# Performance work log

Measured on AMD Instinct MI355X. Metric: run time of the kernel, lower is better.

Reference implementation:

```python
import jax, jax.numpy as jnp
import numpy as np

ITER = 25
SMOOTH = 1e-05


def _maxpool(x, wh, ww):
    # stride-1 'same' max pool over H,W of an NCHW tensor
    return jax.lax.reduce_window(
        x, -jnp.inf, jax.lax.max,
        window_dimensions=(1, 1, wh, ww),
        window_strides=(1, 1, 1, 1),
        padding=[(0, 0), (0, 0), (wh // 2, wh // 2), (ww // 2, ww // 2)])


def soft_erode(img):
    p1 = -_maxpool(-img, 3, 1)
    p2 = -_maxpool(-img, 1, 3)
    return jnp.minimum(p1, p2)


def soft_dilate(img):
    return _maxpool(img, 3, 3)


def soft_open(img):
    return soft_dilate(soft_erode(img))


def soft_skel(img, iter_):
    skel = jax.nn.relu(img - soft_open(img))

    def body(j, carry):
        img, skel = carry
        img = soft_erode(img)
        delta = jax.nn.relu(img - soft_open(img))
        skel = skel + jax.nn.relu(delta - skel * delta)
        return (img, skel)

    _, skel = jax.lax.fori_loop(0, iter_, body, (img, skel))
    return skel


def setup_inputs() -> dict:
    key = jax.random.key(0)
    k1, k2 = jax.random.split(key)
    shape = (32, 1, 1024, 1024)
    target = jax.random.uniform(k1, shape, dtype=jnp.float32)
    inputs = jax.random.uniform(k2, shape, dtype=jnp.float32)
    return {"target": target, "inputs": inputs}


def reference(target, inputs):
    # skeletons computed under no_grad in the original -> stop_gradient
    skel_pred = jax.lax.stop_gradient(soft_skel(inputs, ITER))
    skel_true = jax.lax.stop_gradient(soft_skel(target, ITER))
    tprec = (jnp.sum(skel_pred * target) + SMOOTH) / (jnp.sum(skel_pred) + SMOOTH)
    tsens = (jnp.sum(skel_true * inputs) + SMOOTH) / (jnp.sum(skel_true) + SMOOTH)
    cl_dice = 1.0 - 2.0 * (tprec * tsens) / (tprec + tsens)
    return cl_dice
```

## Files before the change

### kernel.cpp

```cpp
#include <hip/hip_runtime.h>
#include <hip/hip_fp16.h>

#define HH 1024
#define WW 1024
#define NB 32
#define PLANE (HH*WW)
#define RR 118
#define RC 128
typedef unsigned int u32;
typedef unsigned short u16;

static __device__ __forceinline__ u32 pmin(u32 a, u32 b){ u32 d; asm("v_pk_min_f16 %0,%1,%2":"=v"(d):"v"(a),"v"(b)); return d; }
static __device__ __forceinline__ u32 pmax(u32 a, u32 b){ u32 d; asm("v_pk_max_f16 %0,%1,%2":"=v"(d):"v"(a),"v"(b)); return d; }
static __device__ __forceinline__ u32 padd(u32 a, u32 b){ u32 d; asm("v_pk_add_f16 %0,%1,%2":"=v"(d):"v"(a),"v"(b)); return d; }
static __device__ __forceinline__ u32 pmul(u32 a, u32 b){ u32 d; asm("v_pk_mul_f16 %0,%1,%2":"=v"(d):"v"(a),"v"(b)); return d; }
static __device__ __forceinline__ u32 psub(u32 a, u32 b){ u32 d; asm("v_pk_add_f16 %0,%1,%2 neg_lo:[0,1] neg_hi:[0,1]":"=v"(d):"v"(a),"v"(b)); return d; }
static __device__ __forceinline__ float h2f(u32 s){ float f; asm("v_cvt_f32_f16 %0,%1":"=v"(f):"v"(s)); return f; }
static __device__ __forceinline__ u32 cvt2(float a, float b){
    typedef __fp16 h2v __attribute__((ext_vector_type(2)));
    union { h2v h; u32 u; } r; r.h = __builtin_amdgcn_cvt_pkrtz(a,b); return r.u;
}
#define DPP_SHR1(x) ((u32)__builtin_amdgcn_mov_dpp((int)(x), 0x111, 0xf, 0xf, true))
#define DPP_SHL1(x) ((u32)__builtin_amdgcn_mov_dpp((int)(x), 0x101, 0xf, 0xf, true))
#define QNAN2 0x7e007e00u
#define AB(hi,lo) (((lo)>>16)|((hi)<<16))

__global__ __launch_bounds__(256,4) void cldice_fused(const float* __restrict__ inputs,
                                                      const float* __restrict__ target,
                                                      double* __restrict__ acc) {
    __shared__ __align__(16) u16 buf[RR*RC];
    const int tid = threadIdx.x;
    const int bx = blockIdx.x*64, by = blockIdx.y*64;
    const int img = blockIdx.z >> 5, n = blockIdx.z & 31;
    const float* xsrc = (img==0) ? inputs : target;
    const float* wsrc = (img==0) ? target : inputs;
    const float* im = xsrc + (size_t)n*PLANE;
    const bool interior = (bx>=64 && bx<=896 && by>=64 && by<=896);
    const int r0 = tid>>4, c = tid&15;
    const int gx = bx - 32 + 8*c;
    const bool colok = ((unsigned)gx < (unsigned)WW);

    #pragma unroll
    for (int g = 0; g < 8; g++) {
        int r = r0 + g*16;
        if (r < RR) {
            int gy = by - 27 + r;
            uint4 v;
            if (interior || (colok && (unsigned)gy < (unsigned)HH)) {
                const float* p = im + (size_t)gy*WW + gx;
                float4 f0 = *(const float4*)p, f1 = *(const float4*)(p+4);
                v.x = cvt2(f0.x,f0.y); v.y = cvt2(f0.z,f0.w);
                v.z = cvt2(f1.x,f1.y); v.w = cvt2(f1.z,f1.w);
            } else {
                v = make_uint4(QNAN2,QNAN2,QNAN2,QNAN2);
            }
            *(uint4*)&buf[tid*8 + g*2048] = v;
        }
    }
    __syncthreads();

    u32 sk[2][4] = {{0,0,0,0},{0,0,0,0}};
    const int bc0 = 3456 + (tid>>3)*128 + (tid&7)*8;
    const int bc1 = 3456 + ((tid+256)>>3)*128 + (tid&7)*8;

    #pragma unroll 1
    for (int t = 0; t < 26; t++) {
        uint4 st[8];
        #pragma unroll
        for (int g = 0; g < 8; g++) {
            int r = r0 + g*16;
            bool act = (r >= t+1) & (r <= 116-t);
            if (act) {
                int base = tid*8 + g*2048;
                uint4 up = *(const uint4*)&buf[base-RC];
                uint4 md = *(const uint4*)&buf[base];
                uint4 dn = *(const uint4*)&buf[base+RC];
                u32 lfs = DPP_SHR1(md.w);
                u32 rts = DPP_SHL1(md.x);
                u32 vx = pmin(up.x,dn.x), vy = pmin(up.y,dn.y);
                u32 vz = pmin(up.z,dn.z), vw = pmin(up.w,dn.w);
                u32 B1 = AB(md.y,md.x), B2 = AB(md.z,md.y), B3 = AB(md.w,md.z);
                u32 B4 = (md.w>>16)|(rts<<16);
                u32 M0 = (md.x<<16)|(lfs>>16);
                uint4 e;
                e.x = pmin(pmin(vx,md.x), pmin(M0,B1));
                e.y = pmin(pmin(vy,md.y), pmin(B1,B2));
                e.z = pmin(pmin(vz,md.z), pmin(B2,B3));
                e.w = pmin(pmin(vw,md.w), pmin(B3,B4));
                if (!interior) {
                    int gy = by - 27 + r;
                    if (!(colok && (unsigned)gy < (unsigned)HH))
                        e = make_uint4(QNAN2,QNAN2,QNAN2,QNAN2);
                }
                st[g] = e;
            }
        }
        uint4 xs0 = *(const uint4*)&buf[bc0];
        uint4 xs1 = *(const uint4*)&buf[bc1];
        __syncthreads();
        #pragma unroll
        for (int g = 0; g < 8; g++) {
            int r = r0 + g*16;
            if ((r >= t+1) & (r <= 116-t))
                *(uint4*)&buf[tid*8 + g*2048] = st[g];
        }
        __syncthreads();
        #pragma unroll
        for (int j = 0; j < 2; j++) {
            int base = j ? bc1 : bc0;
            uint4 xs = j ? xs1 : xs0;
            uint4 up = *(const uint4*)&buf[base-RC];
            uint4 md = *(const uint4*)&buf[base];
            uint4 dn = *(const uint4*)&buf[base+RC];
            uint4 vm;
            vm.x = pmax(pmax(up.x,dn.x),md.x);
            vm.y = pmax(pmax(up.y,dn.y),md.y);
            vm.z = pmax(pmax(up.z,dn.z),md.z);
            vm.w = pmax(pmax(up.w,dn.w),md.w);
            u32 lfm = DPP_SHR1(vm.w);
            u32 rtm = DPP_SHL1(vm.x);
            if ((tid&7)==0) {
                u32 a = buf[base-RC-1], b = buf[base-1], d2 = buf[base+RC-1];
                lfm = pmax(pmax(a,b),d2) << 16;
            }
            if ((tid&7)==7) {
                u32 a = buf[base-RC+8], b = buf[base+8], d2 = buf[base+RC+8];
                rtm = pmax(pmax(a,b),d2) & 0xffffu;
            }
            u32 B1 = AB(vm.y,vm.x), B2 = AB(vm.z,vm.y), B3 = AB(vm.w,vm.z);
            u32 B4 = (vm.w>>16)|(rtm<<16);
            u32 M0 = (vm.x<<16)|(lfm>>16);
            uint4 d;
            d.x = pmax(pmax(M0,B1), vm.x);
            d.y = pmax(pmax(B1,B2), vm.y);
            d.z = pmax(pmax(B2,B3), vm.z);
            d.w = pmax(pmax(B3,B4), vm.w);
            uint4 dl;
            dl.x = pmax(psub(xs.x,d.x), 0u);
            dl.y = pmax(psub(xs.y,d.y), 0u);
            dl.z = pmax(psub(xs.z,d.z), 0u);
            dl.w = pmax(psub(xs.w,d.w), 0u);
            sk[j][0] = padd(sk[j][0], pmax(psub(dl.x, pmul(sk[j][0],dl.x)), 0u));
            sk[j][1] = padd(sk[j][1], pmax(psub(dl.y, pmul(sk[j][1],dl.y)), 0u));
            sk[j][2] = padd(sk[j][2], pmax(psub(dl.z, pmul(sk[j][2],dl.z)), 0u));
            sk[j][3] = padd(sk[j][3], pmax(psub(dl.w, pmul(sk[j][3],dl.w)), 0u));
        }
    }

    double s0 = 0.0, s1 = 0.0;
    const float* wim = wsrc + (size_t)n*PLANE;
    #pragma unroll
    for (int j = 0; j < 2; j++) {
        int ti = tid + j*256, ty = ti>>3, cx = ti&7;
        const float* p = wim + (size_t)(by+ty)*WW + bx + 8*cx;
        float4 w0 = *(const float4*)p, w1 = *(const float4*)(p+4);
        float f0 = h2f(sk[j][0]&0xffffu), f1 = h2f(sk[j][0]>>16);
        float f2 = h2f(sk[j][1]&0xffffu), f3 = h2f(sk[j][1]>>16);
        float f4 = h2f(sk[j][2]&0xffffu), f5 = h2f(sk[j][2]>>16);
        float f6 = h2f(sk[j][3]&0xffffu), f7 = h2f(sk[j][3]>>16);
        s0 += (double)(f0*w0.x) + (double)(f1*w0.y) + (double)(f2*w0.z) + (double)(f3*w0.w)
            + (double)(f4*w1.x) + (double)(f5*w1.y) + (double)(f6*w1.z) + (double)(f7*w1.w);
        s1 += (double)f0 + (double)f1 + (double)f2 + (double)f3
            + (double)f4 + (double)f5 + (double)f6 + (double)f7;
    }
    #pragma unroll
    for (int off = 32; off > 0; off >>= 1) {
        s0 += __shfl_down(s0, off, 64);
        s1 += __shfl_down(s1, off, 64);
    }
    __syncthreads();
    double* sh = (double*)buf;
    int lane = tid & 63, wid = tid >> 6;
    if (lane == 0) { sh[wid] = s0; sh[4+wid] = s1; }
    __syncthreads();
    if (tid == 0) {
        atomicAdd(&acc[img*2 + 0], sh[0]+sh[1]+sh[2]+sh[3]);
        atomicAdd(&acc[img*2 + 1], sh[4]+sh[5]+sh[6]+sh[7]);
    }
}

__global__ void final_kernel(const double* __restrict__ acc, float* __restrict__ out) {
    double tprec = (acc[0] + 1e-5) / (acc[1] + 1e-5);
    double tsens = (acc[2] + 1e-5) / (acc[3] + 1e-5);
    out[0] = (float)(1.0 - 2.0 * (tprec * tsens) / (tprec + tsens));
}

extern "C" void kernel_launch(void* const* d_in, const int* in_sizes, int n_in,
                              void* d_out, int out_size, void* d_ws, size_t ws_size,
                              hipStream_t stream) {
    const float* target = (const float*)d_in[0];
    const float* inputs = (const float*)d_in[1];
    float* out = (float*)d_out;
    double* acc = (double*)d_ws;

    (void)hipMemsetAsync(acc, 0, 4*sizeof(double), stream);
    dim3 grid(WW/64, HH/64, NB*2);
    cldice_fused<<<grid, dim3(256), 0, stream>>>(inputs, target, acc);
    final_kernel<<<1, 1, 0, stream>>>(acc, out);
}
```

Before: 1.241 ms.

## Double tile height to 128 rows and pad LDS row stride

Grows each block's tile from 64 to 128 output rows, so the 27-row halo on each side is amortized over twice as many outputs and redundant erosion work per pixel drops. The shared-memory row stride is padded to 136 elements, which should reduce bank conflicts. Each thread now keeps 12 staged rows and 4 skeleton accumulators. Launch bounds drop to 3 blocks per CU, trading occupancy and register pressure for less halo recomputation.

```diff
diff --git a/kernel.cpp b/kernel.cpp
--- a/kernel.cpp
+++ b/kernel.cpp
@@ -5,8 +5,8 @@
 #define WW 1024
 #define NB 32
 #define PLANE (HH*WW)
-#define RR 118
-#define RC 128
+#define RR 182
+#define CS 136
 typedef unsigned int u32;
 typedef unsigned short u16;
 
@@ -25,23 +25,24 @@
 #define QNAN2 0x7e007e00u
 #define AB(hi,lo) (((lo)>>16)|((hi)<<16))
 
-__global__ __launch_bounds__(256,4) void cldice_fused(const float* __restrict__ inputs,
+__global__ __launch_bounds__(256,3) void cldice_fused(const float* __restrict__ inputs,
                                                       const float* __restrict__ target,
                                                       double* __restrict__ acc) {
-    __shared__ __align__(16) u16 buf[RR*RC];
+    __shared__ __align__(16) u16 buf[RR*CS];
     const int tid = threadIdx.x;
-    const int bx = blockIdx.x*64, by = blockIdx.y*64;
+    const int bx = blockIdx.x*64, by = blockIdx.y*128;
     const int img = blockIdx.z >> 5, n = blockIdx.z & 31;
     const float* xsrc = (img==0) ? inputs : target;
     const float* wsrc = (img==0) ? target : inputs;
     const float* im = xsrc + (size_t)n*PLANE;
-    const bool interior = (bx>=64 && bx<=896 && by>=64 && by<=896);
+    const bool interior = (bx>=64 && bx<=896 && by>=128 && by<=768);
     const int r0 = tid>>4, c = tid&15;
     const int gx = bx - 32 + 8*c;
     const bool colok = ((unsigned)gx < (unsigned)WW);
-
-    #pragma unroll
-    for (int g = 0; g < 8; g++) {
+    const int rowoff = r0*CS + c*8;
+
+    #pragma unroll
+    for (int g = 0; g < 12; g++) {
         int r = r0 + g*16;
         if (r < RR) {
             int gy = by - 27 + r;
@@ -54,27 +55,31 @@
             } else {
                 v = make_uint4(QNAN2,QNAN2,QNAN2,QNAN2);
             }
-            *(uint4*)&buf[tid*8 + g*2048] = v;
+            *(uint4*)&buf[rowoff + g*16*CS] = v;
         }
     }
     __syncthreads();
 
-    u32 sk[2][4] = {{0,0,0,0},{0,0,0,0}};
-    const int bc0 = 3456 + (tid>>3)*128 + (tid&7)*8;
-    const int bc1 = 3456 + ((tid+256)>>3)*128 + (tid&7)*8;
+    u32 sk[4][4] = {{0,0,0,0},{0,0,0,0},{0,0,0,0},{0,0,0,0}};
+    int bc[4];
+    #pragma unroll
+    for (int j = 0; j < 4; j++) {
+        int ti = tid + j*256;
+        bc[j] = (27 + (ti>>3))*CS + (4 + (ti&7))*8;
+    }
 
     #pragma unroll 1
     for (int t = 0; t < 26; t++) {
-        uint4 st[8];
-        #pragma unroll
-        for (int g = 0; g < 8; g++) {
+        uint4 st[12];
+        #pragma unroll
+        for (int g = 0; g < 12; g++) {
             int r = r0 + g*16;
-            bool act = (r >= t+1) & (r <= 116-t);
+            bool act = (r >= t+1) & (r <= 180-t);
             if (act) {
-                int base = tid*8 + g*2048;
-                uint4 up = *(const uint4*)&buf[base-RC];
+                int base = rowoff + g*16*CS;
+                uint4 up = *(const uint4*)&buf[base-CS];
                 uint4 md = *(const uint4*)&buf[base];
-                uint4 dn = *(const uint4*)&buf[base+RC];
+                uint4 dn = *(const uint4*)&buf[base+CS];
                 u32 lfs = DPP_SHR1(md.w);
                 u32 rts = DPP_SHL1(md.x);
                 u32 vx = pmin(up.x,dn.x), vy = pmin(up.y,dn.y);
@@ -95,23 +100,23 @@
                 st[g] = e;
             }
         }
-        uint4 xs0 = *(const uint4*)&buf[bc0];
-        uint4 xs1 = *(const uint4*)&buf[bc1];
+        uint4 xs[4];
+        #pragma unroll
+        for (int j = 0; j < 4; j++) xs[j] = *(const uint4*)&buf[bc[j]];
         __syncthreads();
         #pragma unroll
-        for (int g = 0; g < 8; g++) {
+        for (int g = 0; g < 12; g++) {
             int r = r0 + g*16;
-            if ((r >= t+1) & (r <= 116-t))
-                *(uint4*)&buf[tid*8 + g*2048] = st[g];
+            if ((r >= t+1) & (r <= 180-t))
+                *(uint4*)&buf[rowoff + g*16*CS] = st[g];
         }
         __syncthreads();
         #pragma unroll
-        for (int j = 0; j < 2; j++) {
-            int base = j ? bc1 : bc0;
-            uint4 xs = j ? xs1 : xs0;
-            uint4 up = *(const uint4*)&buf[base-RC];
+        for (int j = 0; j < 4; j++) {
+            int base = bc[j];
+            uint4 up = *(const uint4*)&buf[base-CS];
             uint4 md = *(const uint4*)&buf[base];
-            uint4 dn = *(const uint4*)&buf[base+RC];
+            uint4 dn = *(const uint4*)&buf[base+CS];
             uint4 vm;
             vm.x = pmax(pmax(up.x,dn.x),md.x);
             vm.y = pmax(pmax(up.y,dn.y),md.y);
@@ -120,11 +125,11 @@
             u32 lfm = DPP_SHR1(vm.w);
             u32 rtm = DPP_SHL1(vm.x);
             if ((tid&7)==0) {
-                u32 a = buf[base-RC-1], b = buf[base-1], d2 = buf[base+RC-1];
+                u32 a = buf[base-CS-1], b = buf[base-1], d2 = buf[base+CS-1];
                 lfm = pmax(pmax(a,b),d2) << 16;
             }
             if ((tid&7)==7) {
-                u32 a = buf[base-RC+8], b = buf[base+8], d2 = buf[base+RC+8];
+                u32 a = buf[base-CS+8], b = buf[base+8], d2 = buf[base+CS+8];
                 rtm = pmax(pmax(a,b),d2) & 0xffffu;
             }
             u32 B1 = AB(vm.y,vm.x), B2 = AB(vm.z,vm.y), B3 = AB(vm.w,vm.z);
@@ -136,10 +141,10 @@
             d.z = pmax(pmax(B2,B3), vm.z);
             d.w = pmax(pmax(B3,B4), vm.w);
             uint4 dl;
-            dl.x = pmax(psub(xs.x,d.x), 0u);
-            dl.y = pmax(psub(xs.y,d.y), 0u);
-            dl.z = pmax(psub(xs.z,d.z), 0u);
-            dl.w = pmax(psub(xs.w,d.w), 0u);
+            dl.x = pmax(psub(xs[j].x,d.x), 0u);
+            dl.y = pmax(psub(xs[j].y,d.y), 0u);
+            dl.z = pmax(psub(xs[j].z,d.z), 0u);
+            dl.w = pmax(psub(xs[j].w,d.w), 0u);
             sk[j][0] = padd(sk[j][0], pmax(psub(dl.x, pmul(sk[j][0],dl.x)), 0u));
             sk[j][1] = padd(sk[j][1], pmax(psub(dl.y, pmul(sk[j][1],dl.y)), 0u));
             sk[j][2] = padd(sk[j][2], pmax(psub(dl.z, pmul(sk[j][2],dl.z)), 0u));
@@ -150,7 +155,7 @@
     double s0 = 0.0, s1 = 0.0;
     const float* wim = wsrc + (size_t)n*PLANE;
     #pragma unroll
-    for (int j = 0; j < 2; j++) {
+    for (int j = 0; j < 4; j++) {
         int ti = tid + j*256, ty = ti>>3, cx = ti&7;
         const float* p = wim + (size_t)(by+ty)*WW + bx + 8*cx;
         float4 w0 = *(const float4*)p, w1 = *(const float4*)(p+4);
@@ -194,7 +199,7 @@
     double* acc = (double*)d_ws;
 
     (void)hipMemsetAsync(acc, 0, 4*sizeof(double), stream);
-    dim3 grid(WW/64, HH/64, NB*2);
+    dim3 grid(WW/64, HH/128, NB*2);
     cldice_fused<<<grid, dim3(256), 0, stream>>>(inputs, target, acc);
     final_kernel<<<1, 1, 0, stream>>>(acc, out);
 }
```

New measurement: 1.263 ms. No clear change (+1.8%).

## Keep erosion tile in registers and exchange only halo rows through LDS

Applied to the files above, without the earlier changes.

Each thread now holds an 8-row strip of the fp16 tile in registers. Only the boundary rows of each strip go through a small double-buffered LDS exchange, which replaces the full-tile shared buffer and one of the two barriers per iteration. The tile grows to 128 output rows with 384 threads, so the vertical halo costs less relative to the useful work. The dilate/skeleton step skips the horizontal halo columns, which frees those threads from that work. The price is higher register pressure (x, e and sk arrays) at 3 blocks per CU, which risks spills or lower occupancy.

```diff
diff --git a/kernel.cpp b/kernel.cpp
--- a/kernel.cpp
+++ b/kernel.cpp
@@ -1,14 +1,10 @@
 #include <hip/hip_runtime.h>
-#include <hip/hip_fp16.h>
 
 #define HH 1024
 #define WW 1024
 #define NB 32
 #define PLANE (HH*WW)
-#define RR 118
-#define RC 128
 typedef unsigned int u32;
-typedef unsigned short u16;
 
 static __device__ __forceinline__ u32 pmin(u32 a, u32 b){ u32 d; asm("v_pk_min_f16 %0,%1,%2":"=v"(d):"v"(a),"v"(b)); return d; }
 static __device__ __forceinline__ u32 pmax(u32 a, u32 b){ u32 d; asm("v_pk_max_f16 %0,%1,%2":"=v"(d):"v"(a),"v"(b)); return d; }
@@ -24,144 +20,142 @@
 #define DPP_SHL1(x) ((u32)__builtin_amdgcn_mov_dpp((int)(x), 0x101, 0xf, 0xf, true))
 #define QNAN2 0x7e007e00u
 #define AB(hi,lo) (((lo)>>16)|((hi)<<16))
+#define QN4 make_uint4(QNAN2,QNAN2,QNAN2,QNAN2)
 
-__global__ __launch_bounds__(256,4) void cldice_fused(const float* __restrict__ inputs,
+static __device__ __forceinline__ uint4 erode_row(uint4 up, uint4 md, uint4 dn){
+    u32 lfs = DPP_SHR1(md.w);
+    u32 rts = DPP_SHL1(md.x);
+    u32 vx = pmin(up.x,dn.x), vy = pmin(up.y,dn.y);
+    u32 vz = pmin(up.z,dn.z), vw = pmin(up.w,dn.w);
+    u32 B1 = AB(md.y,md.x), B2 = AB(md.z,md.y), B3 = AB(md.w,md.z);
+    u32 B4 = (md.w>>16)|(rts<<16);
+    u32 M0 = (md.x<<16)|(lfs>>16);
+    uint4 e;
+    e.x = pmin(pmin(vx,md.x), pmin(M0,B1));
+    e.y = pmin(pmin(vy,md.y), pmin(B1,B2));
+    e.z = pmin(pmin(vz,md.z), pmin(B2,B3));
+    e.w = pmin(pmin(vw,md.w), pmin(B3,B4));
+    return e;
+}
+
+__global__ __launch_bounds__(384,3) void cldice_fused(const float* __restrict__ inputs,
                                                       const float* __restrict__ target,
                                                       double* __restrict__ acc) {
-    __shared__ __align__(16) u16 buf[RR*RC];
+    __shared__ uint4 ex[2][24][2][16];
     const int tid = threadIdx.x;
-    const int bx = blockIdx.x*64, by = blockIdx.y*64;
+    const int s = tid >> 4, c = tid & 15;
+    const int bx = blockIdx.x*64, by = blockIdx.y*128;
     const int img = blockIdx.z >> 5, n = blockIdx.z & 31;
     const float* xsrc = (img==0) ? inputs : target;
     const float* wsrc = (img==0) ? target : inputs;
     const float* im = xsrc + (size_t)n*PLANE;
-    const bool interior = (bx>=64 && bx<=896 && by>=64 && by<=896);
-    const int r0 = tid>>4, c = tid&15;
     const int gx = bx - 32 + 8*c;
     const bool colok = ((unsigned)gx < (unsigned)WW);
+    const int rbase = 8*s;
+    const bool skelcol = (c >= 4 && c <= 11);
 
+    uint4 x[10], e[8], sk[8];
+    bool nok[8];
     #pragma unroll
-    for (int g = 0; g < 8; g++) {
-        int r = r0 + g*16;
-        if (r < RR) {
-            int gy = by - 27 + r;
-            uint4 v;
-            if (interior || (colok && (unsigned)gy < (unsigned)HH)) {
-                const float* p = im + (size_t)gy*WW + gx;
-                float4 f0 = *(const float4*)p, f1 = *(const float4*)(p+4);
-                v.x = cvt2(f0.x,f0.y); v.y = cvt2(f0.z,f0.w);
-                v.z = cvt2(f1.x,f1.y); v.w = cvt2(f1.z,f1.w);
-            } else {
-                v = make_uint4(QNAN2,QNAN2,QNAN2,QNAN2);
-            }
-            *(uint4*)&buf[tid*8 + g*2048] = v;
-        }
+    for (int k = 0; k < 10; k++) {
+        int r = rbase - 1 + k, gy = by - 27 + r;
+        if (colok && r >= 0 && r <= 181 && gy >= 0 && gy < HH) {
+            const float* p = im + (size_t)gy*WW + gx;
+            float4 f0 = *(const float4*)p, f1 = *(const float4*)(p+4);
+            x[k].x = cvt2(f0.x,f0.y); x[k].y = cvt2(f0.z,f0.w);
+            x[k].z = cvt2(f1.x,f1.y); x[k].w = cvt2(f1.z,f1.w);
+        } else x[k] = QN4;
     }
-    __syncthreads();
-
-    u32 sk[2][4] = {{0,0,0,0},{0,0,0,0}};
-    const int bc0 = 3456 + (tid>>3)*128 + (tid&7)*8;
-    const int bc1 = 3456 + ((tid+256)>>3)*128 + (tid&7)*8;
+    #pragma unroll
+    for (int i = 0; i < 8; i++) {
+        int r = rbase + i, gy = by - 27 + r;
+        nok[i] = !(colok && r <= 181 && gy >= 0 && gy < HH);
+        e[i] = QN4;
+        sk[i] = make_uint4(0,0,0,0);
+    }
 
     #pragma unroll 1
     for (int t = 0; t < 26; t++) {
-        uint4 st[8];
         #pragma unroll
-        for (int g = 0; g < 8; g++) {
-            int r = r0 + g*16;
-            bool act = (r >= t+1) & (r <= 116-t);
-            if (act) {
-                int base = tid*8 + g*2048;
-                uint4 up = *(const uint4*)&buf[base-RC];
-                uint4 md = *(const uint4*)&buf[base];
-                uint4 dn = *(const uint4*)&buf[base+RC];
-                u32 lfs = DPP_SHR1(md.w);
-                u32 rts = DPP_SHL1(md.x);
-                u32 vx = pmin(up.x,dn.x), vy = pmin(up.y,dn.y);
-                u32 vz = pmin(up.z,dn.z), vw = pmin(up.w,dn.w);
-                u32 B1 = AB(md.y,md.x), B2 = AB(md.z,md.y), B3 = AB(md.w,md.z);
-                u32 B4 = (md.w>>16)|(rts<<16);
-                u32 M0 = (md.x<<16)|(lfs>>16);
-                uint4 e;
-                e.x = pmin(pmin(vx,md.x), pmin(M0,B1));
-                e.y = pmin(pmin(vy,md.y), pmin(B1,B2));
-                e.z = pmin(pmin(vz,md.z), pmin(B2,B3));
-                e.w = pmin(pmin(vw,md.w), pmin(B3,B4));
-                if (!interior) {
-                    int gy = by - 27 + r;
-                    if (!(colok && (unsigned)gy < (unsigned)HH))
-                        e = make_uint4(QNAN2,QNAN2,QNAN2,QNAN2);
-                }
-                st[g] = e;
+        for (int i = 0; i < 8; i++) {
+            int r = rbase + i;
+            if (r >= t+1 && r <= 180-t) {
+                uint4 ev = erode_row(x[i], x[i+1], x[i+2]);
+                if (nok[i]) ev = QN4;
+                e[i] = ev;
             }
         }
-        uint4 xs0 = *(const uint4*)&buf[bc0];
-        uint4 xs1 = *(const uint4*)&buf[bc1];
+        uint4 (*exb)[2][16] = ex[t&1];
+        exb[s][0][c] = e[0];
+        exb[s][1][c] = e[7];
         __syncthreads();
+        uint4 xm1 = (s > 0)  ? exb[s-1][1][c] : QN4;
+        uint4 xp8 = (s < 23) ? exb[s+1][0][c] : QN4;
         #pragma unroll
-        for (int g = 0; g < 8; g++) {
-            int r = r0 + g*16;
-            if ((r >= t+1) & (r <= 116-t))
-                *(uint4*)&buf[tid*8 + g*2048] = st[g];
+        for (int i = 0; i < 8; i++) {
+            int r = rbase + i;
+            if (r >= 27 && r <= 154) {
+                uint4 em = (i == 0) ? xm1 : e[i-1];
+                uint4 ep = (i == 7) ? xp8 : e[i+1];
+                uint4 ec = e[i];
+                uint4 vm;
+                vm.x = pmax(pmax(em.x,ep.x),ec.x);
+                vm.y = pmax(pmax(em.y,ep.y),ec.y);
+                vm.z = pmax(pmax(em.z,ep.z),ec.z);
+                vm.w = pmax(pmax(em.w,ep.w),ec.w);
+                u32 lfm = DPP_SHR1(vm.w);
+                u32 rtm = DPP_SHL1(vm.x);
+                if (skelcol) {
+                    u32 B1 = AB(vm.y,vm.x), B2 = AB(vm.z,vm.y), B3 = AB(vm.w,vm.z);
+                    u32 B4 = (vm.w>>16)|(rtm<<16);
+                    u32 M0 = (vm.x<<16)|(lfm>>16);
+                    uint4 d;
+                    d.x = pmax(pmax(M0,B1), vm.x);
+                    d.y = pmax(pmax(B1,B2), vm.y);
+                    d.z = pmax(pmax(B2,B3), vm.z);
+                    d.w = pmax(pmax(B3,B4), vm.w);
+                    uint4 xs = x[i+1];
+                    uint4 dl;
+                    dl.x = pmax(psub(xs.x,d.x), 0u);
+                    dl.y = pmax(psub(xs.y,d.y), 0u);
+                    dl.z = pmax(psub(xs.z,d.z), 0u);
+                    dl.w = pmax(psub(xs.w,d.w), 0u);
+                    sk[i].x = padd(sk[i].x, pmax(psub(dl.x, pmul(sk[i].x,dl.x)), 0u));
+                    sk[i].y = padd(sk[i].y, pmax(psub(dl.y, pmul(sk[i].y,dl.y)), 0u));
+                    sk[i].z = padd(sk[i].z, pmax(psub(dl.z, pmul(sk[i].z,dl.z)), 0u));
+                    sk[i].w = padd(sk[i].w, pmax(psub(dl.w, pmul(sk[i].w,dl.w)), 0u));
+                }
+            }
         }
-        __syncthreads();
+        x[0] = xm1;
         #pragma unroll
-        for (int j = 0; j < 2; j++) {
-            int base = j ? bc1 : bc0;
-            uint4 xs = j ? xs1 : xs0;
-            uint4 up = *(const uint4*)&buf[base-RC];
-            uint4 md = *(const uint4*)&buf[base];
-            uint4 dn = *(const uint4*)&buf[base+RC];
-            uint4 vm;
-            vm.x = pmax(pmax(up.x,dn.x),md.x);
-            vm.y = pmax(pmax(up.y,dn.y),md.y);
-            vm.z = pmax(pmax(up.z,dn.z),md.z);
-            vm.w = pmax(pmax(up.w,dn.w),md.w);
-            u32 lfm = DPP_SHR1(vm.w);
-            u32 rtm = DPP_SHL1(vm.x);
-            if ((tid&7)==0) {
-                u32 a = buf[base-RC-1], b = buf[base-1], d2 = buf[base+RC-1];
-                lfm = pmax(pmax(a,b),d2) << 16;
-            }
-            if ((tid&7)==7) {
-                u32 a = buf[base-RC+8], b = buf[base+8], d2 = buf[base+RC+8];
-                rtm = pmax(pmax(a,b),d2) & 0xffffu;
-            }
-            u32 B1 = AB(vm.y,vm.x), B2 = AB(vm.z,vm.y), B3 = AB(vm.w,vm.z);
-            u32 B4 = (vm.w>>16)|(rtm<<16);
-            u32 M0 = (vm.x<<16)|(lfm>>16);
-            uint4 d;
-            d.x = pmax(pmax(M0,B1), vm.x);
-            d.y = pmax(pmax(B1,B2), vm.y);
-            d.z = pmax(pmax(B2,B3), vm.z);
-            d.w = pmax(pmax(B3,B4), vm.w);
-            uint4 dl;
-            dl.x = pmax(psub(xs.x,d.x), 0u);
-            dl.y = pmax(psub(xs.y,d.y), 0u);
-            dl.z = pmax(psub(xs.z,d.z), 0u);
-            dl.w = pmax(psub(xs.w,d.w), 0u);
-            sk[j][0] = padd(sk[j][0], pmax(psub(dl.x, pmul(sk[j][0],dl.x)), 0u));
-            sk[j][1] = padd(sk[j][1], pmax(psub(dl.y, pmul(sk[j][1],dl.y)), 0u));
-            sk[j][2] = padd(sk[j][2], pmax(psub(dl.z, pmul(sk[j][2],dl.z)), 0u));
-            sk[j][3] = padd(sk[j][3], pmax(psub(dl.w, pmul(sk[j][3],dl.w)), 0u));
+        for (int i = 0; i < 8; i++) {
+            int r = rbase + i;
+            if (r >= t+1 && r <= 180-t) x[i+1] = e[i];
         }
+        x[9] = xp8;
     }
 
     double s0 = 0.0, s1 = 0.0;
-    const float* wim = wsrc + (size_t)n*PLANE;
-    #pragma unroll
-    for (int j = 0; j < 2; j++) {
-        int ti = tid + j*256, ty = ti>>3, cx = ti&7;
-        const float* p = wim + (size_t)(by+ty)*WW + bx + 8*cx;
-        float4 w0 = *(const float4*)p, w1 = *(const float4*)(p+4);
-        float f0 = h2f(sk[j][0]&0xffffu), f1 = h2f(sk[j][0]>>16);
-        float f2 = h2f(sk[j][1]&0xffffu), f3 = h2f(sk[j][1]>>16);
-        float f4 = h2f(sk[j][2]&0xffffu), f5 = h2f(sk[j][2]>>16);
-        float f6 = h2f(sk[j][3]&0xffffu), f7 = h2f(sk[j][3]>>16);
-        s0 += (double)(f0*w0.x) + (double)(f1*w0.y) + (double)(f2*w0.z) + (double)(f3*w0.w)
-            + (double)(f4*w1.x) + (double)(f5*w1.y) + (double)(f6*w1.z) + (double)(f7*w1.w);
-        s1 += (double)f0 + (double)f1 + (double)f2 + (double)f3
-            + (double)f4 + (double)f5 + (double)f6 + (double)f7;
+    if (skelcol) {
+        const float* wim = wsrc + (size_t)n*PLANE;
+        #pragma unroll
+        for (int i = 0; i < 8; i++) {
+            int r = rbase + i;
+            if (r >= 27 && r <= 154) {
+                int gy = by - 27 + r;
+                const float* p = wim + (size_t)gy*WW + gx;
+                float4 w0 = *(const float4*)p, w1 = *(const float4*)(p+4);
+                float f0 = h2f(sk[i].x&0xffffu), f1 = h2f(sk[i].x>>16);
+                float f2 = h2f(sk[i].y&0xffffu), f3 = h2f(sk[i].y>>16);
+                float f4 = h2f(sk[i].z&0xffffu), f5 = h2f(sk[i].z>>16);
+                float f6 = h2f(sk[i].w&0xffffu), f7 = h2f(sk[i].w>>16);
+                s0 += (double)(f0*w0.x) + (double)(f1*w0.y) + (double)(f2*w0.z) + (double)(f3*w0.w)
+                    + (double)(f4*w1.x) + (double)(f5*w1.y) + (double)(f6*w1.z) + (double)(f7*w1.w);
+                s1 += (double)f0 + (double)f1 + (double)f2 + (double)f3
+                    + (double)f4 + (double)f5 + (double)f6 + (double)f7;
+            }
+        }
     }
     #pragma unroll
     for (int off = 32; off > 0; off >>= 1) {
@@ -169,13 +163,13 @@
         s1 += __shfl_down(s1, off, 64);
     }
     __syncthreads();
-    double* sh = (double*)buf;
+    double* sh = (double*)ex;
     int lane = tid & 63, wid = tid >> 6;
-    if (lane == 0) { sh[wid] = s0; sh[4+wid] = s1; }
+    if (lane == 0) { sh[wid] = s0; sh[6+wid] = s1; }
     __syncthreads();
     if (tid == 0) {
-        atomicAdd(&acc[img*2 + 0], sh[0]+sh[1]+sh[2]+sh[3]);
-        atomicAdd(&acc[img*2 + 1], sh[4]+sh[5]+sh[6]+sh[7]);
+        atomicAdd(&acc[img*2 + 0], sh[0]+sh[1]+sh[2]+sh[3]+sh[4]+sh[5]);
+        atomicAdd(&acc[img*2 + 1], sh[6]+sh[7]+sh[8]+sh[9]+sh[10]+sh[11]);
     }
 }
 
@@ -194,7 +188,7 @@
     double* acc = (double*)d_ws;
 
     (void)hipMemsetAsync(acc, 0, 4*sizeof(double), stream);
-    dim3 grid(WW/64, HH/64, NB*2);
-    cldice_fused<<<grid, dim3(256), 0, stream>>>(inputs, target, acc);
+    dim3 grid(WW/64, HH/128, NB*2);
+    cldice_fused<<<grid, dim3(384), 0, stream>>>(inputs, target, acc);
     final_kernel<<<1, 1, 0, stream>>>(acc, out);
 }
```

Result: slower. 2.637 ms (+112.4%).
